# Optimization experiments

Hardware: AMD Instinct MI355X
Metric: run time of the kernel (lower is better)

Reference implementation:

```python
import jax, jax.numpy as jnp
import numpy as np

BS, N, D_ENT, K, D_IN, D_F, H, L, S = 128, 512, 256, 128, 1024, 256, 128, 2, 64
MAX_ENTITY_NUM = 512.0
TEMP = 1.0
NEG = -1e9


def _ln(x, g, b, eps=1e-5):
    m = jnp.mean(x, -1, keepdims=True)
    v = jnp.mean((x - m) ** 2, -1, keepdims=True)
    return (x - m) * jax.lax.rsqrt(v + eps) * g + b


def setup_inputs() -> dict:
    key = jax.random.key(0)
    ks = jax.random.split(key, 16)
    nrm = lambda k, sh, s=0.02: jax.random.normal(k, sh, jnp.float32) * s
    entity_num = jax.random.randint(ks[0], (BS,), 64, N)
    selected_units = jax.random.randint(ks[1], (BS, S), 0, N + 1) % (entity_num[:, None] + 1)
    selected_units_num = jax.random.randint(ks[2], (BS,), 1, S + 1).at[0].set(S)  # max == S so torch seq_len == S
    return dict(
        embedding=nrm(ks[3], (BS, D_IN), 1.0),
        entity_embedding=nrm(ks[4], (BS, N, D_ENT), 1.0),
        key_w=nrm(ks[5], (K, D_ENT)), key_b=jnp.zeros((K,), jnp.float32),
        q1_w=nrm(ks[6], (D_F, D_IN)), q1_b=jnp.zeros((D_F,), jnp.float32),
        q2_w=nrm(ks[7], (K, D_F)), q2_b=jnp.zeros((K,), jnp.float32),
        e1_w=nrm(ks[8], (D_F, K)), e1_b=jnp.zeros((D_F,), jnp.float32),
        e2_w=nrm(ks[9], (D_IN, D_F)), e2_b=jnp.zeros((D_IN,), jnp.float32),
        end_embedding=nrm(ks[10], (1, K), 0.09),
        lstm_wih=nrm(ks[11], (L, 4 * H, K)),
        lstm_whh=nrm(ks[12], (L, 4 * H, H)),
        ln_ig=jnp.ones((L, 4 * H), jnp.float32), ln_ib=jnp.zeros((L, 4 * H), jnp.float32),
        ln_hg=jnp.ones((L, 4 * H), jnp.float32), ln_hb=jnp.zeros((L, 4 * H), jnp.float32),
        ln_cg=jnp.ones((L, H), jnp.float32), ln_cb=jnp.zeros((L, H), jnp.float32),
        entity_num=entity_num, selected_units=selected_units, selected_units_num=selected_units_num,
    )


def _forward(embedding, entity_embedding, key_w, key_b, q1_w, q1_b, q2_w, q2_b,
             e1_w, e1_b, e2_w, e2_b, end_embedding, lstm_wih, lstm_whh,
             ln_ig, ln_ib, ln_hg, ln_hb, ln_cg, ln_cb,
             entity_num, selected_units, selected_units_num):
    bs = embedding.shape[0]
    ar = jnp.arange(bs)
    # keys: [bs, N+1, K] with end-embedding placed at position entity_num
    key = jnp.einsum('bnd,kd->bnk', entity_embedding, key_w) + key_b
    key = jnp.concatenate([key, jnp.zeros((bs, 1, K), key.dtype)], axis=1)
    key = key.at[ar, entity_num].set(end_embedding[0])
    # entity_reduce_type == 'constant': key_embeddings = embed_mlp(key / MAX_ENTITY_NUM)
    kr = key / MAX_ENTITY_NUM
    key_emb = jax.nn.relu(jnp.einsum('bnk,fk->bnf', kr, e1_w) + e1_b)
    key_emb = jnp.einsum('bnf,df->bnd', key_emb, e2_w) + e2_b  # [bs, N+1, D_IN]
    # precompute per-step masks (cumulative disabling of previously selected units;
    # end token blocked only at step 0, then re-enabled unless selected)
    init_mask = jnp.arange(N + 1)[None, :] < (entity_num + 1)[:, None]
    oh = jax.nn.one_hot(selected_units, N + 1, dtype=jnp.int32)
    prev = jnp.cumsum(oh, axis=1) - oh  # selected strictly before step i
    mask_seq = init_mask[:, None, :] & (prev == 0)  # [bs, S, N+1]
    mask_seq = mask_seq.at[ar, 0, entity_num].set(False)

    def step(carry, xs):
        ae, hs, cs = carry
        i, su_i, m_i = xs
        # query MLP
        x = jax.nn.relu(ae @ q1_w.T + q1_b) @ q2_w.T + q2_b  # [bs, K]
        new_hs, new_cs = [], []
        for l in range(L):  # layer-norm LSTM stack
            gates = _ln(x @ lstm_wih[l].T, ln_ig[l], ln_ib[l]) + _ln(hs[l] @ lstm_whh[l].T, ln_hg[l], ln_hb[l])
            ig, fg, gg, og = jnp.split(gates, 4, axis=-1)
            c = _ln(jax.nn.sigmoid(fg) * cs[l] + jax.nn.sigmoid(ig) * jnp.tanh(gg), ln_cg[l], ln_cb[l])
            h = jax.nn.sigmoid(og) * jnp.tanh(c)
            new_hs.append(h); new_cs.append(c)
            x = h
        logits = jnp.where(m_i, jnp.einsum('bk,bnk->bn', x, key) / TEMP, NEG)
        gate = ((i + 1) <= selected_units_num) & (su_i != entity_num)
        ae = ae + key_emb[ar, su_i] * gate[:, None].astype(ae.dtype)
        return (ae, jnp.stack(new_hs), jnp.stack(new_cs)), logits

    hs0 = jnp.zeros((L, bs, H), embedding.dtype)
    cs0 = jnp.zeros((L, bs, H), embedding.dtype)
    (ae, _, _), logits = jax.lax.scan(
        step, (embedding, hs0, cs0),
        (jnp.arange(S), selected_units.T, jnp.swapaxes(mask_seq, 0, 1)))
    return jnp.swapaxes(logits, 0, 1), ae  # logits [bs, S, N+1]


def reference(embedding, entity_embedding, key_w, key_b, q1_w, q1_b, q2_w, q2_b,
              e1_w, e1_b, e2_w, e2_b, end_embedding, lstm_wih, lstm_whh,
              ln_ig, ln_ib, ln_hg, ln_hb, ln_cg, ln_cb,
              entity_num, selected_units, selected_units_num):
    logits, ae = _forward(embedding, entity_embedding, key_w, key_b, q1_w, q1_b, q2_w, q2_b,
                          e1_w, e1_b, e2_w, e2_b, end_embedding, lstm_wih, lstm_whh,
                          ln_ig, ln_ib, ln_hg, ln_hb, ln_cg, ln_cb,
                          entity_num, selected_units, selected_units_num)
    # torch forward returns (logits, units=None, embedding, selected_units_num); units omitted here
    return logits, ae, selected_units_num
```

## Files before the change

### kernel.cpp

```cpp
#include <hip/hip_runtime.h>
#include <hip/hip_bf16.h>
#include <math.h>

#define BSZ   128
#define NENT  512
#define NP1   513
#define DENT  256
#define KDIM  128
#define DIN   1024
#define DF    256
#define HDIM  128
#define SSTEP 64
#define G4    512
#define NEGV  (-1e9f)
#define INV_MAX (1.0f/512.0f)

typedef float v2f __attribute__((ext_vector_type(2)));
typedef __attribute__((ext_vector_type(8))) short bf16x8;
typedef __attribute__((ext_vector_type(4))) float f32x4;

__device__ inline float sigf(float x){ return 1.f/(1.f+__expf(-x)); }
__device__ inline float tanh_fast(float x){ float e=__expf(2.f*x); return 1.f - 2.f/(e+1.f); }

__device__ inline float sum16_partial(float x){
  x += __int_as_float(__builtin_amdgcn_update_dpp(0, __float_as_int(x), 0x111, 0xf, 0xf, true));
  x += __int_as_float(__builtin_amdgcn_update_dpp(0, __float_as_int(x), 0x112, 0xf, 0xf, true));
  x += __int_as_float(__builtin_amdgcn_update_dpp(0, __float_as_int(x), 0x114, 0xf, 0xf, true));
  x += __int_as_float(__builtin_amdgcn_update_dpp(0, __float_as_int(x), 0x118, 0xf, 0xf, true));
  return x;
}
__device__ inline float wave_sum_partial(float x){
  x = sum16_partial(x);
  x += __int_as_float(__builtin_amdgcn_update_dpp(0, __float_as_int(x), 0x142, 0xa, 0xf, true));
  x += __int_as_float(__builtin_amdgcn_update_dpp(0, __float_as_int(x), 0x143, 0xc, 0xf, true));
  return x;
}
__device__ inline float wave_sum(float x){
  return __int_as_float(__builtin_amdgcn_readlane(__float_as_int(wave_sum_partial(x)), 63));
}

__device__ inline unsigned pk8(float4 f){
  int r = 0;
  r = __builtin_amdgcn_cvt_pk_fp8_f32(f.x, f.y, r, false);
  r = __builtin_amdgcn_cvt_pk_fp8_f32(f.z, f.w, r, true);
  return (unsigned)r;
}
__device__ inline float dot4_fp8(unsigned w, float4 h, float acc){
  v2f p = __builtin_amdgcn_cvt_pk_f32_fp8((int)w, false);
  acc = fmaf(p.x, h.x, acc); acc = fmaf(p.y, h.y, acc);
  p = __builtin_amdgcn_cvt_pk_f32_fp8((int)w, true);
  acc = fmaf(p.x, h.z, acc); acc = fmaf(p.y, h.w, acc);
  return acc;
}

__device__ inline float2 block_reduce2(float x, float y, float* red){
  float sx0 = wave_sum_partial(x), sy0 = wave_sum_partial(y);
  int w = threadIdx.x>>6;
  __syncthreads();
  if((threadIdx.x&63)==63){ red[w]=sx0; red[8+w]=sy0; }
  __syncthreads();
  float sx=0.f, sy=0.f;
  #pragma unroll
  for(int q=0;q<8;q++){ sx+=red[q]; sy+=red[8+q]; }
  return make_float2(sx,sy);
}

template<bool BKMAJOR, bool RELU, bool GATHER>
__global__ __launch_bounds__(256)
void mfma_gemm(const float* __restrict__ A, const float* __restrict__ B,
               const float* __restrict__ bias, float* __restrict__ C,
               int M, int N, int K,
               const int* __restrict__ gidx, float scale){
  __shared__ ushort Abf[64][72];
  __shared__ ushort Bbf[64][72];
  const int t = threadIdx.x;
  const int bm = blockIdx.x, bn = blockIdx.y;
  const int w = t>>6, l = t&63;
  const int lm = l&15, lg = l>>4;
  const int r0 = w*16;
  f32x4 acc[4];
  #pragma unroll
  for(int f=0;f<4;f++) acc[f] = (f32x4){0.f,0.f,0.f,0.f};

  for(int k0=0;k0<K;k0+=64){
    #pragma unroll
    for(int i=0;i<4;i++){
      int idx = t + i*256;
      int row = idx>>4, c4 = (idx&15)<<2;
      const float* src;
      if(GATHER){
        int gr = bm*64+row;
        src = &A[((size_t)(gr>>6)*NP1 + gidx[gr])*(size_t)K + k0 + c4];
      } else {
        src = &A[((size_t)bm*64+row)*K + k0 + c4];
      }
      float4 v = *(const float4*)src;
      if(GATHER){ v.x*=scale; v.y*=scale; v.z*=scale; v.w*=scale; }
      ushort4 u;
      u.x = __float_as_uint(v.x)>>16; u.y = __float_as_uint(v.y)>>16;
      u.z = __float_as_uint(v.z)>>16; u.w = __float_as_uint(v.w)>>16;
      *(ushort4*)&Abf[row][c4] = u;
    }
    if(!BKMAJOR){
      #pragma unroll
      for(int i=0;i<4;i++){
        int idx = t + i*256;
        int row = idx>>4, c4 = (idx&15)<<2;
        float4 v = *(const float4*)&B[((size_t)bn*64+row)*K + k0 + c4];
        ushort4 u;
        u.x = __float_as_uint(v.x)>>16; u.y = __float_as_uint(v.y)>>16;
        u.z = __float_as_uint(v.z)>>16; u.w = __float_as_uint(v.w)>>16;
        *(ushort4*)&Bbf[row][c4] = u;
      }
    } else {
      #pragma unroll
      for(int i=0;i<4;i++){
        int idx = t + i*256;
        int kr = idx>>4, n4 = (idx&15)<<2;
        float4 v = *(const float4*)&B[(size_t)(k0+kr)*N + bn*64 + n4];
        Bbf[n4+0][kr] = __float_as_uint(v.x)>>16;
        Bbf[n4+1][kr] = __float_as_uint(v.y)>>16;
        Bbf[n4+2][kr] = __float_as_uint(v.z)>>16;
        Bbf[n4+3][kr] = __float_as_uint(v.w)>>16;
      }
    }
    __syncthreads();
    #pragma unroll
    for(int kk=0;kk<64;kk+=32){
      bf16x8 a = *(const bf16x8*)&Abf[r0+lm][kk + lg*8];
      #pragma unroll
      for(int f=0;f<4;f++){
        bf16x8 b = *(const bf16x8*)&Bbf[f*16+lm][kk + lg*8];
        acc[f] = __builtin_amdgcn_mfma_f32_16x16x32_bf16(a, b, acc[f], 0,0,0);
      }
    }
    __syncthreads();
  }
  #pragma unroll
  for(int f=0;f<4;f++){
    int gcol = bn*64 + f*16 + lm;
    float bb = bias ? bias[gcol] : 0.f;
    #pragma unroll
    for(int r=0;r<4;r++){
      int grow = bm*64 + r0 + lg*4 + r;
      float v = acc[f][r] + bb;
      if(RELU) v = fmaxf(v, 0.f);
      C[(size_t)grow*N + gcol] = v;
    }
  }
}

__global__ __launch_bounds__(256)
void key_gemm_mfma(const float* __restrict__ A, const float* __restrict__ W,
                   const float* __restrict__ bias, const int* __restrict__ en,
                   const float* __restrict__ end_emb, float* __restrict__ C){
  __shared__ ushort Abf[64][264];
  __shared__ ushort Bbf[128][264];
  __shared__ float bs[128];
  const int t = threadIdx.x;
  const int bm = blockIdx.x;
  #pragma unroll
  for(int i=0;i<16;i++){
    int idx = t + i*256;
    int row = idx>>6, c4 = (idx&63)<<2;
    float4 v = *(const float4*)&A[((size_t)bm*64+row)*256 + c4];
    ushort4 u;
    u.x = __float_as_uint(v.x)>>16; u.y = __float_as_uint(v.y)>>16;
    u.z = __float_as_uint(v.z)>>16; u.w = __float_as_uint(v.w)>>16;
    *(ushort4*)&Abf[row][c4] = u;
  }
  #pragma unroll
  for(int i=0;i<32;i++){
    int idx = t + i*256;
    int row = idx>>6, c4 = (idx&63)<<2;
    float4 v = *(const float4*)&W[(size_t)row*256 + c4];
    ushort4 u;
    u.x = __float_as_uint(v.x)>>16; u.y = __float_as_uint(v.y)>>16;
    u.z = __float_as_uint(v.z)>>16; u.w = __float_as_uint(v.w)>>16;
    *(ushort4*)&Bbf[row][c4] = u;
  }
  if(t<128) bs[t] = bias[t];
  __syncthreads();
  const int w = t>>6, l = t&63;
  const int lm = l&15, lg = l>>4;
  const int r0 = w*16;
  f32x4 acc[8];
  #pragma unroll
  for(int f=0;f<8;f++) acc[f] = (f32x4){0.f,0.f,0.f,0.f};
  #pragma unroll
  for(int k0=0;k0<256;k0+=32){
    bf16x8 a = *(const bf16x8*)&Abf[r0+lm][k0 + lg*8];
    #pragma unroll
    for(int f=0;f<8;f++){
      bf16x8 b = *(const bf16x8*)&Bbf[f*16+lm][k0 + lg*8];
      acc[f] = __builtin_amdgcn_mfma_f32_16x16x32_bf16(a, b, acc[f], 0,0,0);
    }
  }
  #pragma unroll
  for(int f=0;f<8;f++){
    int gcol = f*16 + lm;
    float bb = bs[gcol];
    float ev = end_emb[gcol];
    #pragma unroll
    for(int r=0;r<4;r++){
      int grow = bm*64 + r0 + lg*4 + r;
      int bq = grow>>9, n = grow&511;
      size_t orow = (size_t)bq*NP1 + n;
      float v = acc[f][r] + bb;
      if(n == en[bq]) v = ev;
      C[orow*KDIM + gcol] = v;
    }
  }
}

__global__ __launch_bounds__(256)
void g0_gemm_ln(const float* __restrict__ X, const float* __restrict__ W,
                const float* __restrict__ gam, const float* __restrict__ bet,
                float* __restrict__ G0){
  __shared__ ushort Abf[16][136];
  __shared__ float redS[16][4], redQ[16][4];
  const int t = threadIdx.x, bm = blockIdx.x;
  const int w = t>>6, l = t&63, lm = l&15, lg = l>>4;
  {
    int idx = t*8;
    int row = idx>>7, c = idx&127;
    const float* src = &X[((size_t)bm*16+row)*128 + c];
    float4 a = *(const float4*)src;
    float4 d = *(const float4*)(src+4);
    ushort4 u0, u1;
    u0.x=__float_as_uint(a.x)>>16; u0.y=__float_as_uint(a.y)>>16;
    u0.z=__float_as_uint(a.z)>>16; u0.w=__float_as_uint(a.w)>>16;
    u1.x=__float_as_uint(d.x)>>16; u1.y=__float_as_uint(d.y)>>16;
    u1.z=__float_as_uint(d.z)>>16; u1.w=__float_as_uint(d.w)>>16;
    *(ushort4*)&Abf[row][c] = u0;
    *(ushort4*)&Abf[row][c+4] = u1;
  }
  __syncthreads();
  f32x4 acc[8];
  #pragma unroll
  for(int f=0;f<8;f++) acc[f] = (f32x4){0.f,0.f,0.f,0.f};
  #pragma unroll
  for(int kt=0;kt<4;kt++){
    int k0 = kt*32;
    bf16x8 a = *(const bf16x8*)&Abf[lm][k0 + lg*8];
    #pragma unroll
    for(int f=0;f<8;f++){
      int brow = w*128 + f*16 + lm;
      const float* bp = &W[(size_t)brow*128 + k0 + lg*8];
      float4 b0 = *(const float4*)bp;
      float4 b1 = *(const float4*)(bp+4);
      bf16x8 bfr;
      bfr[0]=(short)(__float_as_uint(b0.x)>>16); bfr[1]=(short)(__float_as_uint(b0.y)>>16);
      bfr[2]=(short)(__float_as_uint(b0.z)>>16); bfr[3]=(short)(__float_as_uint(b0.w)>>16);
      bfr[4]=(short)(__float_as_uint(b1.x)>>16); bfr[5]=(short)(__float_as_uint(b1.y)>>16);
      bfr[6]=(short)(__float_as_uint(b1.z)>>16); bfr[7]=(short)(__float_as_uint(b1.w)>>16);
      acc[f] = __builtin_amdgcn_mfma_f32_16x16x32_bf16(a, bfr, acc[f], 0,0,0);
    }
  }
  float mu[4], rs[4];
  #pragma unroll
  for(int r=0;r<4;r++){
    float s=0.f, q=0.f;
    #pragma unroll
    for(int f=0;f<8;f++){ float x=acc[f][r]; s+=x; q+=x*x; }
    s = sum16_partial(s);
    q = sum16_partial(q);
    if(lm==15){ redS[lg*4+r][w]=s; redQ[lg*4+r][w]=q; }
  }
  __syncthreads();
  #pragma unroll
  for(int r=0;r<4;r++){
    int row = lg*4+r;
    float S = redS[row][0]+redS[row][1]+redS[row][2]+redS[row][3];
    float Q = redQ[row][0]+redQ[row][1]+redQ[row][2]+redQ[row][3];
    mu[r] = S*(1.f/512.f);
    rs[r] = rsqrtf(Q*(1.f/512.f) - mu[r]*mu[r] + 1e-5f);
  }
  #pragma unroll
  for(int f=0;f<8;f++){
    int col = w*128 + f*16 + lm;
    float g = gam[col], bt = bet[col];
    #pragma unroll
    for(int r=0;r<4;r++){
      int grow = bm*16 + lg*4 + r;
      G0[(size_t)grow*G4 + col] = (acc[f][r]-mu[r])*rs[r]*g + bt;
    }
  }
}

__global__ __launch_bounds__(256)
void c0_kernel(const float* __restrict__ q1_w, const float* __restrict__ e2_b,
               float* __restrict__ c0v){
  __shared__ float red[4];
  int f = blockIdx.x, t = threadIdx.x;
  float4 a = *(const float4*)&q1_w[(size_t)f*DIN + t*4];
  float4 e = *(const float4*)&e2_b[t*4];
  float p = a.x*e.x + a.y*e.y + a.z*e.z + a.w*e.w;
  float s = wave_sum_partial(p);
  if((t&63)==63) red[t>>6] = s;
  __syncthreads();
  if(t==0) c0v[f] = red[0]+red[1]+red[2]+red[3];
}

__global__ void prefix_kernel(const float* __restrict__ U0, const float* __restrict__ Q1K,
                              const float* __restrict__ c0v, const float* __restrict__ T1,
                              const int* __restrict__ su, const int* __restrict__ en,
                              const int* __restrict__ sun,
                              float* __restrict__ RU, float* __restrict__ s1,
                              float* __restrict__ ngout){
  int b = blockIdx.x, f = threadIdx.x;
  float acc = U0[b*DF+f];
  float c0f = c0v[f];
  float s1a = 0.f, ng = 0.f;
  int enb = en[b], sunb = sun[b];
  for(int j=0;j<SSTEP;j++){
    int r = b*SSTEP+j;
    float q = Q1K[(size_t)r*DF+f];
    float tt = T1[(size_t)r*DF+f];
    RU[(size_t)r*DF+f] = fmaxf(acc,0.f);
    int sj = su[r];
    float g = ((j+1)<=sunb && sj!=enb) ? 1.f : 0.f;
    acc = fmaf(g, q + c0f, acc);
    s1a = fmaf(g, tt, s1a);
    ng += g;
  }
  s1[b*DF+f]=s1a;
  if(f==0) ngout[b]=ng;
}

__global__ __launch_bounds__(512)
__attribute__((amdgpu_waves_per_eu(2,2)))
void lstm_serial(const float* __restrict__ wih, const float* __restrict__ whh,
                 const float* __restrict__ G0,
                 const float* __restrict__ ln_ig, const float* __restrict__ ln_ib,
                 const float* __restrict__ ln_hg, const float* __restrict__ ln_hb,
                 const float* __restrict__ ln_cg, const float* __restrict__ ln_cb,
                 float* __restrict__ H1){
  const int b = blockIdx.x;
  const int j = threadIdx.x;
  __shared__ uint4 W0s8[8][512];
  __shared__ uint4 W1s8[8][512];
  __shared__ float h0s[128], h1s[128];
  __shared__ float pvv[512], pv1[512];
  __shared__ float lnA[512], lnB[512], lnC[512], lnD[512], lnE[512], lnF[512];
  __shared__ float red[32];

  #pragma unroll
  for(int c=0;c<8;c++){
    const float* s0 = &whh[(size_t)j*KDIM + c*16];
    uint4 p;
    p.x = pk8(*(const float4*)(s0+ 0));
    p.y = pk8(*(const float4*)(s0+ 4));
    p.z = pk8(*(const float4*)(s0+ 8));
    p.w = pk8(*(const float4*)(s0+12));
    W0s8[c][j] = p;
    const float* s1 = &wih[65536 + (size_t)j*KDIM + c*16];
    uint4 q;
    q.x = pk8(*(const float4*)(s1+ 0));
    q.y = pk8(*(const float4*)(s1+ 4));
    q.z = pk8(*(const float4*)(s1+ 8));
    q.w = pk8(*(const float4*)(s1+12));
    W1s8[c][j] = q;
  }
  uint4 w2p[8];
  #pragma unroll
  for(int c=0;c<8;c++){
    const float* s2 = &whh[65536 + (size_t)j*KDIM + c*16];
    w2p[c].x = pk8(*(const float4*)(s2+ 0));
    w2p[c].y = pk8(*(const float4*)(s2+ 4));
    w2p[c].z = pk8(*(const float4*)(s2+ 8));
    w2p[c].w = pk8(*(const float4*)(s2+12));
  }
  lnA[j] = ln_hg[j];     lnB[j] = ln_hb[j];
  lnC[j] = ln_ig[512+j]; lnD[j] = ln_ib[512+j];
  lnE[j] = ln_hg[512+j]; lnF[j] = ln_hb[512+j];

  float cg0A=0.f,cb0A=0.f,cg0B=0.f,cb0B=0.f;
  float cg1A=0.f,cb1A=0.f,cg1B=0.f,cb1B=0.f;
  float c0rA=0.f,c0rB=0.f,c1rA=0.f,c1rB=0.f;
  if(j<64){
    cg0A=ln_cg[j];      cb0A=ln_cb[j];
    cg0B=ln_cg[j+64];   cb0B=ln_cb[j+64];
    cg1A=ln_cg[128+j];    cb1A=ln_cb[128+j];
    cg1B=ln_cg[128+j+64]; cb1B=ln_cb[128+j+64];
  }
  if(j<128){ h0s[j]=0.f; h1s[j]=0.f; }
  __syncthreads();

  const float4* h04 = (const float4*)h0s;
  const float4* h14 = (const float4*)h1s;
  const int w = j>>6;

  for(int i=0;i<SSTEP;i++){
    float g0a[4], g0b[4];
    if(j<64){
      const float* gp = &G0[((size_t)b*SSTEP+i)*G4];
      #pragma unroll
      for(int k=0;k<4;k++){ g0a[k]=gp[j+128*k]; g0b[k]=gp[j+64+128*k]; }
    }

    float v = 0.f, vb = 0.f;
    #pragma unroll
    for(int c=0;c<8;c++){
      uint4 ww = W0s8[c][j];
      v  = dot4_fp8(ww.x, h04[4*c+0], v );
      vb = dot4_fp8(ww.y, h04[4*c+1], vb);
      v  = dot4_fp8(ww.z, h04[4*c+2], v );
      vb = dot4_fp8(ww.w, h04[4*c+3], vb);
    }
    v += vb;
    float v1 = 0.f, v1b = 0.f;
    #pragma unroll
    for(int c=0;c<8;c++){
      uint4 ww = w2p[c];
      v1  = dot4_fp8(ww.x, h14[4*c+0], v1 );
      v1b = dot4_fp8(ww.y, h14[4*c+1], v1b);
      v1  = dot4_fp8(ww.z, h14[4*c+2], v1 );
      v1b = dot4_fp8(ww.w, h14[4*c+3], v1b);
    }
    v1 += v1b;
    {
      float a  = wave_sum_partial(v);
      float bq = wave_sum_partial(v*v);
      float c2 = wave_sum_partial(v1);
      float d  = wave_sum_partial(v1*v1);
      if((j&63)==63){ red[w]=a; red[8+w]=bq; red[16+w]=c2; red[24+w]=d; }
    }
    pvv[j]=v; pv1[j]=v1;
    __syncthreads();

    if(j<64){
      float S=0.f,S2=0.f;
      #pragma unroll
      for(int q=0;q<8;q++){ S+=red[q]; S2+=red[8+q]; }
      float mu = S*(1.f/512.f);
      float rs = rsqrtf(S2*(1.f/512.f) - mu*mu + 1e-5f);
      float ashA[4], ashB[4];
      #pragma unroll
      for(int k=0;k<4;k++){
        int ia = j + 128*k, ib = j + 64 + 128*k;
        ashA[k] = g0a[k] + (pvv[ia]-mu)*rs*lnA[ia] + lnB[ia];
        ashB[k] = g0b[k] + (pvv[ib]-mu)*rs*lnA[ib] + lnB[ib];
      }
      float cpA = sigf(ashA[1])*c0rA + sigf(ashA[0])*tanh_fast(ashA[2]);
      float cpB = sigf(ashB[1])*c0rB + sigf(ashB[0])*tanh_fast(ashB[2]);
      float s  = wave_sum(cpA+cpB);
      float s2 = wave_sum(cpA*cpA+cpB*cpB);
      float muc = s*(1.f/128.f);
      float rsc = rsqrtf(s2*(1.f/128.f) - muc*muc + 1e-5f);
      c0rA = (cpA-muc)*rsc*cg0A + cb0A;
      c0rB = (cpB-muc)*rsc*cg0B + cb0B;
      h0s[j]    = sigf(ashA[3])*tanh_fast(c0rA);
      h0s[j+64] = sigf(ashB[3])*tanh_fast(c0rB);
    }
    __syncthreads();

    float u = 0.f, ub = 0.f;
    #pragma unroll
    for(int c=0;c<8;c++){
      uint4 ww = W1s8[c][j];
      u  = dot4_fp8(ww.x, h04[4*c+0], u );
      ub = dot4_fp8(ww.y, h04[4*c+1], ub);
      u  = dot4_fp8(ww.z, h04[4*c+2], u );
      ub = dot4_fp8(ww.w, h04[4*c+3], ub);
    }
    u += ub;
    {
      float a  = wave_sum_partial(u);
      float bq = wave_sum_partial(u*u);
      if((j&63)==63){ red[w]=a; red[8+w]=bq; }
    }
    pvv[j]=u;
    __syncthreads();

    if(j<64){
      float Su=0.f,Su2=0.f,Sv=0.f,Sv2=0.f;
      #pragma unroll
      for(int q=0;q<8;q++){ Su+=red[q]; Su2+=red[8+q]; Sv+=red[16+q]; Sv2+=red[24+q]; }
      float muu = Su*(1.f/512.f);
      float rsu = rsqrtf(Su2*(1.f/512.f) - muu*muu + 1e-5f);
      float muv = Sv*(1.f/512.f);
      float rsv = rsqrtf(Sv2*(1.f/512.f) - muv*muv + 1e-5f);
      float ashA[4], ashB[4];
      #pragma unroll
      for(int k=0;k<4;k++){
        int ia = j + 128*k, ib = j + 64 + 128*k;
        ashA[k] = (pvv[ia]-muu)*rsu*lnC[ia] + lnD[ia]
                + (pv1[ia]-muv)*rsv*lnE[ia] + lnF[ia];
        ashB[k] = (pvv[ib]-muu)*rsu*lnC[ib] + lnD[ib]
                + (pv1[ib]-muv)*rsv*lnE[ib] + lnF[ib];
      }
      float cpA = sigf(ashA[1])*c1rA + sigf(ashA[0])*tanh_fast(ashA[2]);
      float cpB = sigf(ashB[1])*c1rB + sigf(ashB[0])*tanh_fast(ashB[2]);
      float s  = wave_sum(cpA+cpB);
      float s2 = wave_sum(cpA*cpA+cpB*cpB);
      float muc = s*(1.f/128.f);
      float rsc = rsqrtf(s2*(1.f/128.f) - muc*muc + 1e-5f);
      c1rA = (cpA-muc)*rsc*cg1A + cb1A;
      c1rB = (cpB-muc)*rsc*cg1B + cb1B;
      float hA = sigf(ashA[3])*tanh_fast(c1rA);
      float hB = sigf(ashB[3])*tanh_fast(c1rB);
      h1s[j]    = hA;
      h1s[j+64] = hB;
      H1[((size_t)b*SSTEP+i)*HDIM + j]      = hA;
      H1[((size_t)b*SSTEP+i)*HDIM + j + 64] = hB;
    }
    __syncthreads();
  }
}

__global__ __launch_bounds__(512)
void logits_kernel(const float* __restrict__ key, const float* __restrict__ H1,
                   const int* __restrict__ en, const int* __restrict__ su,
                   float* __restrict__ out){
  const int b = blockIdx.x;
  const int ihalf = blockIdx.y;
  __shared__ float HsT[128][36];
  __shared__ int firstsel[NP1];
  for(int t=threadIdx.x; t<32*HDIM; t+=512){
    int il = t>>7, k = t&127;
    HsT[k][il] = H1[(size_t)b*SSTEP*HDIM + (size_t)(ihalf*32+il)*HDIM + k];
  }
  for(int t=threadIdx.x; t<NP1; t+=512) firstsel[t] = 1<<30;
  __syncthreads();
  if(threadIdx.x < SSTEP) atomicMin(&firstsel[su[b*SSTEP+threadIdx.x]], (int)threadIdx.x);
  __syncthreads();
  const int enb = en[b];
  const int tn = threadIdx.x & 255;
  const int ig = threadIdx.x >> 8;
  const int i0l = ig*16;
  const int ig0 = ihalf*32 + i0l;
  float acc0[16], acc1[16];
  #pragma unroll
  for(int q=0;q<16;q++){ acc0[q]=0.f; acc1[q]=0.f; }
  const float* kr0 = key + ((size_t)b*NP1 + tn)*KDIM;
  const float* kr1 = key + ((size_t)b*NP1 + tn + 256)*KDIM;
  for(int k=0;k<KDIM;k+=4){
    float4 kv0 = *(const float4*)&kr0[k];
    float4 kv1 = *(const float4*)&kr1[k];
    float k0a[4] = {kv0.x,kv0.y,kv0.z,kv0.w};
    float k1a[4] = {kv1.x,kv1.y,kv1.z,kv1.w};
    #pragma unroll
    for(int kk=0;kk<4;kk++){
      float4 h0 = *(const float4*)&HsT[k+kk][i0l+0];
      float4 h1 = *(const float4*)&HsT[k+kk][i0l+4];
      float4 h2 = *(const float4*)&HsT[k+kk][i0l+8];
      float4 h3 = *(const float4*)&HsT[k+kk][i0l+12];
      float ka = k0a[kk], kb = k1a[kk];
      acc0[ 0]=fmaf(ka,h0.x,acc0[ 0]); acc0[ 1]=fmaf(ka,h0.y,acc0[ 1]);
      acc0[ 2]=fmaf(ka,h0.z,acc0[ 2]); acc0[ 3]=fmaf(ka,h0.w,acc0[ 3]);
      acc0[ 4]=fmaf(ka,h1.x,acc0[ 4]); acc0[ 5]=fmaf(ka,h1.y,acc0[ 5]);
      acc0[ 6]=fmaf(ka,h1.z,acc0[ 6]); acc0[ 7]=fmaf(ka,h1.w,acc0[ 7]);
      acc0[ 8]=fmaf(ka,h2.x,acc0[ 8]); acc0[ 9]=fmaf(ka,h2.y,acc0[ 9]);
      acc0[10]=fmaf(ka,h2.z,acc0[10]); acc0[11]=fmaf(ka,h2.w,acc0[11]);
      acc0[12]=fmaf(ka,h3.x,acc0[12]); acc0[13]=fmaf(ka,h3.y,acc0[13]);
      acc0[14]=fmaf(ka,h3.z,acc0[14]); acc0[15]=fmaf(ka,h3.w,acc0[15]);
      acc1[ 0]=fmaf(kb,h0.x,acc1[ 0]); acc1[ 1]=fmaf(kb,h0.y,acc1[ 1]);
      acc1[ 2]=fmaf(kb,h0.z,acc1[ 2]); acc1[ 3]=fmaf(kb,h0.w,acc1[ 3]);
      acc1[ 4]=fmaf(kb,h1.x,acc1[ 4]); acc1[ 5]=fmaf(kb,h1.y,acc1[ 5]);
      acc1[ 6]=fmaf(kb,h1.z,acc1[ 6]); acc1[ 7]=fmaf(kb,h1.w,acc1[ 7]);
      acc1[ 8]=fmaf(kb,h2.x,acc1[ 8]); acc1[ 9]=fmaf(kb,h2.y,acc1[ 9]);
      acc1[10]=fmaf(kb,h2.z,acc1[10]); acc1[11]=fmaf(kb,h2.w,acc1[11]);
      acc1[12]=fmaf(kb,h3.x,acc1[12]); acc1[13]=fmaf(kb,h3.y,acc1[13]);
      acc1[14]=fmaf(kb,h3.z,acc1[14]); acc1[15]=fmaf(kb,h3.w,acc1[15]);
    }
  }
  const int n0 = tn, n1 = tn + 256;
  const int fs0 = firstsel[n0], fs1 = firstsel[n1];
  #pragma unroll
  for(int q=0;q<16;q++){
    int i = ig0 + q;
    bool m0 = (n0 <= enb) && (fs0 >= i) && !(i==0 && n0==enb);
    bool m1 = (n1 <= enb) && (fs1 >= i) && !(i==0 && n1==enb);
    out[((size_t)b*SSTEP + i)*NP1 + n0] = m0 ? acc0[q] : NEGV;
    out[((size_t)b*SSTEP + i)*NP1 + n1] = m1 ? acc1[q] : NEGV;
  }
  if(threadIdx.x < 32){
    int i = ihalf*32 + threadIdx.x;
    out[((size_t)b*SSTEP + i)*NP1 + 512] = NEGV;
  }
}

__global__ __launch_bounds__(256)
void ae_gemm(const float* __restrict__ A, const float* __restrict__ B,
             const float* __restrict__ emb, const float* __restrict__ e2_b,
             const float* __restrict__ ng, const int* __restrict__ sun,
             float* __restrict__ out){
  const size_t AE_OFF = (size_t)BSZ*SSTEP*NP1;
  const size_t SUN_OFF = AE_OFF + (size_t)BSZ*DIN;
  __shared__ ushort Abf[64][72];
  __shared__ ushort Bbf[64][72];
  const int t = threadIdx.x;
  const int bm = blockIdx.x, bn = blockIdx.y;
  const int w = t>>6, l = t&63;
  const int lm = l&15, lg = l>>4;
  const int r0 = w*16;
  f32x4 acc[4];
  #pragma unroll
  for(int f=0;f<4;f++) acc[f] = (f32x4){0.f,0.f,0.f,0.f};
  for(int k0=0;k0<256;k0+=64){
    #pragma unroll
    for(int i=0;i<4;i++){
      int idx = t + i*256;
      int row = idx>>4, c4 = (idx&15)<<2;
      float4 v = *(const float4*)&A[((size_t)bm*64+row)*256 + k0 + c4];
      ushort4 u;
      u.x = __float_as_uint(v.x)>>16; u.y = __float_as_uint(v.y)>>16;
      u.z = __float_as_uint(v.z)>>16; u.w = __float_as_uint(v.w)>>16;
      *(ushort4*)&Abf[row][c4] = u;
    }
    #pragma unroll
    for(int i=0;i<4;i++){
      int idx = t + i*256;
      int row = idx>>4, c4 = (idx&15)<<2;
      float4 v = *(const float4*)&B[((size_t)bn*64+row)*256 + k0 + c4];
      ushort4 u;
      u.x = __float_as_uint(v.x)>>16; u.y = __float_as_uint(v.y)>>16;
      u.z = __float_as_uint(v.z)>>16; u.w = __float_as_uint(v.w)>>16;
      *(ushort4*)&Bbf[row][c4] = u;
    }
    __syncthreads();
    #pragma unroll
    for(int kk=0;kk<64;kk+=32){
      bf16x8 a = *(const bf16x8*)&Abf[r0+lm][kk + lg*8];
      #pragma unroll
      for(int f=0;f<4;f++){
        bf16x8 b = *(const bf16x8*)&Bbf[f*16+lm][kk + lg*8];
        acc[f] = __builtin_amdgcn_mfma_f32_16x16x32_bf16(a, b, acc[f], 0,0,0);
      }
    }
    __syncthreads();
  }
  #pragma unroll
  for(int f=0;f<4;f++){
    int gcol = bn*64 + f*16 + lm;
    float eb = e2_b[gcol];
    #pragma unroll
    for(int r=0;r<4;r++){
      int grow = bm*64 + r0 + lg*4 + r;
      size_t o = (size_t)grow*DIN + gcol;
      out[AE_OFF + o] = emb[o] + acc[f][r] + ng[grow]*eb;
    }
  }
  if(bm==0 && bn==0 && t<BSZ) out[SUN_OFF + t] = (float)sun[t];
}

extern "C" void kernel_launch(void* const* d_in, const int* in_sizes, int n_in,
                              void* d_out, int out_size, void* d_ws, size_t ws_size,
                              hipStream_t stream){
  const float* emb     = (const float*)d_in[0];
  const float* ent     = (const float*)d_in[1];
  const float* key_w   = (const float*)d_in[2];
  const float* key_b   = (const float*)d_in[3];
  const float* q1_w    = (const float*)d_in[4];
  const float* q1_b    = (const float*)d_in[5];
  const float* q2_w    = (const float*)d_in[6];
  const float* q2_b    = (const float*)d_in[7];
  const float* e1_w    = (const float*)d_in[8];
  const float* e1_b    = (const float*)d_in[9];
  const float* e2_w    = (const float*)d_in[10];
  const float* e2_b    = (const float*)d_in[11];
  const float* end_emb = (const float*)d_in[12];
  const float* wih     = (const float*)d_in[13];
  const float* whh     = (const float*)d_in[14];
  const float* ln_ig   = (const float*)d_in[15];
  const float* ln_ib   = (const float*)d_in[16];
  const float* ln_hg   = (const float*)d_in[17];
  const float* ln_hb   = (const float*)d_in[18];
  const float* ln_cg   = (const float*)d_in[19];
  const float* ln_cb   = (const float*)d_in[20];
  const int* en  = (const int*)d_in[21];
  const int* su  = (const int*)d_in[22];
  const int* sun = (const int*)d_in[23];
  float* out = (float*)d_out;
  float* ws  = (float*)d_ws;

  const size_t o_key = 0;
  const size_t o_T1  = o_key + 8404992;
  const size_t o_q1e = o_T1  + 2097152;
  const size_t o_c0  = o_q1e + 65536;
  const size_t o_U0  = o_c0  + 1024;
  const size_t o_Q1K = o_U0  + 32768;
  const size_t o_RU  = o_Q1K + 2097152;
  const size_t o_X   = o_RU  + 2097152;
  const size_t o_G0  = o_X   + 1048576;
  const size_t o_s1  = o_G0  + 4194304;
  const size_t o_ng  = o_s1  + 32768;
  const size_t o_H1  = o_ng  + 1024;

  key_gemm_mfma<<<1024,256,0,stream>>>(ent, key_w, key_b, en, end_emb, ws+o_key);
  mfma_gemm<false,true,true><<<dim3(128,4),256,0,stream>>>(ws+o_key, e1_w, e1_b, ws+o_T1,
                                                           8192,256,128, su, INV_MAX);
  mfma_gemm<true,false,false><<<dim3(4,4),256,0,stream>>>(q1_w, e2_w, nullptr, ws+o_q1e,
                                                          256,256,1024, nullptr, 1.f);
  c0_kernel<<<256,256,0,stream>>>(q1_w, e2_b, ws+o_c0);
  mfma_gemm<false,false,false><<<dim3(2,4),256,0,stream>>>(emb, q1_w, q1_b, ws+o_U0,
                                                           128,256,1024, nullptr, 1.f);
  mfma_gemm<false,false,false><<<dim3(128,4),256,0,stream>>>(ws+o_T1, ws+o_q1e, nullptr, ws+o_Q1K,
                                                             8192,256,256, nullptr, 1.f);
  prefix_kernel<<<128,256,0,stream>>>(ws+o_U0, ws+o_Q1K, ws+o_c0, ws+o_T1, su, en, sun,
                                      ws+o_RU, ws+o_s1, ws+o_ng);
  mfma_gemm<false,false,false><<<dim3(128,2),256,0,stream>>>(ws+o_RU, q2_w, q2_b, ws+o_X,
                                                             8192,128,256, nullptr, 1.f);
  g0_gemm_ln<<<512,256,0,stream>>>(ws+o_X, wih, ln_ig, ln_ib, ws+o_G0);
  lstm_serial<<<128,512,0,stream>>>(wih, whh, ws+o_G0,
                                    ln_ig, ln_ib, ln_hg, ln_hb, ln_cg, ln_cb, ws+o_H1);
  logits_kernel<<<dim3(128,2),512,0,stream>>>(ws+o_key, ws+o_H1, en, su, out);
  ae_gemm<<<dim3(2,16),256,0,stream>>>(ws+o_s1, e2_w, emb, e2_b, ws+o_ng, sun, out);
}
```

Before: 529.7 us.

## Use fp8 MFMA for serial LSTM recurrent matvecs with fp8 hidden state

Replaces the per-thread scalar fp8 dot products in the serial LSTM kernel with 16x16x32 fp8 MFMA instructions. The hidden vector is quantized to fp8 and placed in row 0 of the A operand, with the other rows zeroed. Weights are re-laid out in shared memory and registers to match the MFMA B-operand fragments. The goal is fewer VALU ops on the latency-bound recurrent step. In exchange, 15 of 16 MFMA rows are wasted, and quantizing the hidden state to fp8 lowers accuracy.

```diff
diff --git a/kernel.cpp b/kernel.cpp
--- a/kernel.cpp
+++ b/kernel.cpp
@@ -18,6 +18,7 @@
 typedef float v2f __attribute__((ext_vector_type(2)));
 typedef __attribute__((ext_vector_type(8))) short bf16x8;
 typedef __attribute__((ext_vector_type(4))) float f32x4;
+typedef long i64;
 
 __device__ inline float sigf(float x){ return 1.f/(1.f+__expf(-x)); }
 __device__ inline float tanh_fast(float x){ float e=__expf(2.f*x); return 1.f - 2.f/(e+1.f); }
@@ -45,13 +46,7 @@
   r = __builtin_amdgcn_cvt_pk_fp8_f32(f.z, f.w, r, true);
   return (unsigned)r;
 }
-__device__ inline float dot4_fp8(unsigned w, float4 h, float acc){
-  v2f p = __builtin_amdgcn_cvt_pk_f32_fp8((int)w, false);
-  acc = fmaf(p.x, h.x, acc); acc = fmaf(p.y, h.y, acc);
-  p = __builtin_amdgcn_cvt_pk_f32_fp8((int)w, true);
-  acc = fmaf(p.x, h.z, acc); acc = fmaf(p.y, h.w, acc);
-  return acc;
-}
+__device__ inline i64 u2l(uint2 v){ union{uint2 u; i64 l;} x; x.u=v; return x.l; }
 
 __device__ inline float2 block_reduce2(float x, float y, float* red){
   float sx0 = wave_sum_partial(x), sy0 = wave_sum_partial(y);
@@ -338,38 +333,43 @@
                  float* __restrict__ H1){
   const int b = blockIdx.x;
   const int j = threadIdx.x;
-  __shared__ uint4 W0s8[8][512];
-  __shared__ uint4 W1s8[8][512];
-  __shared__ float h0s[128], h1s[128];
+  const int w = j>>6, l = j&63;
+  const int lm = l&15, lg = l>>4;
+  __shared__ uint2 W0f[4][4][512];
+  __shared__ uint2 W1f[4][4][512];
+  __shared__ uint4 h0q8[8], h1q8[8];
   __shared__ float pvv[512], pv1[512];
   __shared__ float lnA[512], lnB[512], lnC[512], lnD[512], lnE[512], lnF[512];
   __shared__ float red[32];
 
-  #pragma unroll
-  for(int c=0;c<8;c++){
-    const float* s0 = &whh[(size_t)j*KDIM + c*16];
-    uint4 p;
-    p.x = pk8(*(const float4*)(s0+ 0));
-    p.y = pk8(*(const float4*)(s0+ 4));
-    p.z = pk8(*(const float4*)(s0+ 8));
-    p.w = pk8(*(const float4*)(s0+12));
-    W0s8[c][j] = p;
-    const float* s1 = &wih[65536 + (size_t)j*KDIM + c*16];
-    uint4 q;
-    q.x = pk8(*(const float4*)(s1+ 0));
-    q.y = pk8(*(const float4*)(s1+ 4));
-    q.z = pk8(*(const float4*)(s1+ 8));
-    q.w = pk8(*(const float4*)(s1+12));
-    W1s8[c][j] = q;
-  }
-  uint4 w2p[8];
-  #pragma unroll
-  for(int c=0;c<8;c++){
-    const float* s2 = &whh[65536 + (size_t)j*KDIM + c*16];
-    w2p[c].x = pk8(*(const float4*)(s2+ 0));
-    w2p[c].y = pk8(*(const float4*)(s2+ 4));
-    w2p[c].z = pk8(*(const float4*)(s2+ 8));
-    w2p[c].w = pk8(*(const float4*)(s2+12));
+  {
+    unsigned dw[32];
+    #pragma unroll
+    for(int q=0;q<32;q++) dw[q] = pk8(*(const float4*)&whh[(size_t)j*KDIM + q*4]);
+    #pragma unroll
+    for(int kt=0;kt<4;kt++)
+      #pragma unroll
+      for(int g=0;g<4;g++)
+        W0f[kt][g][j] = make_uint2(dw[kt*8+g*2], dw[kt*8+g*2+1]);
+    #pragma unroll
+    for(int q=0;q<32;q++) dw[q] = pk8(*(const float4*)&wih[65536 + (size_t)j*KDIM + q*4]);
+    #pragma unroll
+    for(int kt=0;kt<4;kt++)
+      #pragma unroll
+      for(int g=0;g<4;g++)
+        W1f[kt][g][j] = make_uint2(dw[kt*8+g*2], dw[kt*8+g*2+1]);
+  }
+  uint2 w2f[4][4];
+  #pragma unroll
+  for(int c=0;c<4;c++){
+    int row = w*64 + c*16 + lm;
+    #pragma unroll
+    for(int kt=0;kt<4;kt++){
+      int k0 = kt*32 + lg*8;
+      float4 x0 = *(const float4*)&whh[65536 + (size_t)row*KDIM + k0];
+      float4 x1 = *(const float4*)&whh[65536 + (size_t)row*KDIM + k0 + 4];
+      w2f[c][kt] = make_uint2(pk8(x0), pk8(x1));
+    }
   }
   lnA[j] = ln_hg[j];     lnB[j] = ln_hb[j];
   lnC[j] = ln_ig[512+j]; lnD[j] = ln_ib[512+j];
@@ -384,12 +384,10 @@
     cg1A=ln_cg[128+j];    cb1A=ln_cb[128+j];
     cg1B=ln_cg[128+j+64]; cb1B=ln_cb[128+j+64];
   }
-  if(j<128){ h0s[j]=0.f; h1s[j]=0.f; }
-  __syncthreads();
-
-  const float4* h04 = (const float4*)h0s;
-  const float4* h14 = (const float4*)h1s;
-  const int w = j>>6;
+  if(j<8){ h0q8[j]=(uint4){0,0,0,0}; h1q8[j]=(uint4){0,0,0,0}; }
+  __syncthreads();
+
+  const int colbase = w*64;
 
   for(int i=0;i<SSTEP;i++){
     float g0a[4], g0b[4];
@@ -399,34 +397,43 @@
       for(int k=0;k<4;k++){ g0a[k]=gp[j+128*k]; g0b[k]=gp[j+64+128*k]; }
     }
 
-    float v = 0.f, vb = 0.f;
-    #pragma unroll
-    for(int c=0;c<8;c++){
-      uint4 ww = W0s8[c][j];
-      v  = dot4_fp8(ww.x, h04[4*c+0], v );
-      vb = dot4_fp8(ww.y, h04[4*c+1], vb);
-      v  = dot4_fp8(ww.z, h04[4*c+2], v );
-      vb = dot4_fp8(ww.w, h04[4*c+3], vb);
-    }
-    v += vb;
-    float v1 = 0.f, v1b = 0.f;
-    #pragma unroll
-    for(int c=0;c<8;c++){
-      uint4 ww = w2p[c];
-      v1  = dot4_fp8(ww.x, h14[4*c+0], v1 );
-      v1b = dot4_fp8(ww.y, h14[4*c+1], v1b);
-      v1  = dot4_fp8(ww.z, h14[4*c+2], v1 );
-      v1b = dot4_fp8(ww.w, h14[4*c+3], v1b);
-    }
-    v1 += v1b;
+    f32x4 accv[4], acc1[4];
+    #pragma unroll
+    for(int c=0;c<4;c++){ accv[c]=(f32x4){0.f,0.f,0.f,0.f}; acc1[c]=(f32x4){0.f,0.f,0.f,0.f}; }
+    #pragma unroll
+    for(int kt=0;kt<4;kt++){
+      uint2 a0 = make_uint2(0,0), a1 = make_uint2(0,0);
+      if(lm==0){
+        a0 = *(const uint2*)((const char*)h0q8 + kt*32 + lg*8);
+        a1 = *(const uint2*)((const char*)h1q8 + kt*32 + lg*8);
+      }
+      i64 A0 = u2l(a0), A1 = u2l(a1);
+      #pragma unroll
+      for(int c=0;c<4;c++){
+        accv[c] = __builtin_amdgcn_mfma_f32_16x16x32_fp8_fp8(A0, u2l(W0f[kt][lg][colbase+c*16+lm]), accv[c], 0,0,0);
+        acc1[c] = __builtin_amdgcn_mfma_f32_16x16x32_fp8_fp8(A1, u2l(w2f[c][kt]), acc1[c], 0,0,0);
+      }
+    }
     {
-      float a  = wave_sum_partial(v);
-      float bq = wave_sum_partial(v*v);
-      float c2 = wave_sum_partial(v1);
-      float d  = wave_sum_partial(v1*v1);
-      if((j&63)==63){ red[w]=a; red[8+w]=bq; red[16+w]=c2; red[24+w]=d; }
-    }
-    pvv[j]=v; pv1[j]=v1;
+      float sv=0.f, sq=0.f, s1v=0.f, s1q=0.f;
+      #pragma unroll
+      for(int c=0;c<4;c++){
+        float x = accv[c][0]; sv += x; sq += x*x;
+        float y = acc1[c][0]; s1v += y; s1q += y*y;
+      }
+      float a  = wave_sum_partial(sv);
+      float bq = wave_sum_partial(sq);
+      float c2 = wave_sum_partial(s1v);
+      float d  = wave_sum_partial(s1q);
+      if(l==63){ red[w]=a; red[8+w]=bq; red[16+w]=c2; red[24+w]=d; }
+      if(l<16){
+        #pragma unroll
+        for(int c=0;c<4;c++){
+          pvv[colbase + c*16 + l] = accv[c][0];
+          pv1[colbase + c*16 + l] = acc1[c][0];
+        }
+      }
+    }
     __syncthreads();
 
     if(j<64){
@@ -450,27 +457,38 @@
       float rsc = rsqrtf(s2*(1.f/128.f) - muc*muc + 1e-5f);
       c0rA = (cpA-muc)*rsc*cg0A + cb0A;
       c0rB = (cpB-muc)*rsc*cg0B + cb0B;
-      h0s[j]    = sigf(ashA[3])*tanh_fast(c0rA);
-      h0s[j+64] = sigf(ashB[3])*tanh_fast(c0rB);
+      float hA = sigf(ashA[3])*tanh_fast(c0rA);
+      float hB = sigf(ashB[3])*tanh_fast(c0rB);
+      ((unsigned char*)h0q8)[j]    = (unsigned char)(__builtin_amdgcn_cvt_pk_fp8_f32(hA,hA,0,false)&0xff);
+      ((unsigned char*)h0q8)[j+64] = (unsigned char)(__builtin_amdgcn_cvt_pk_fp8_f32(hB,hB,0,false)&0xff);
     }
     __syncthreads();
 
-    float u = 0.f, ub = 0.f;
-    #pragma unroll
-    for(int c=0;c<8;c++){
-      uint4 ww = W1s8[c][j];
-      u  = dot4_fp8(ww.x, h04[4*c+0], u );
-      ub = dot4_fp8(ww.y, h04[4*c+1], ub);
-      u  = dot4_fp8(ww.z, h04[4*c+2], u );
-      ub = dot4_fp8(ww.w, h04[4*c+3], ub);
-    }
-    u += ub;
+    f32x4 accu[4];
+    #pragma unroll
+    for(int c=0;c<4;c++) accu[c]=(f32x4){0.f,0.f,0.f,0.f};
+    #pragma unroll
+    for(int kt=0;kt<4;kt++){
+      uint2 a0 = make_uint2(0,0);
+      if(lm==0) a0 = *(const uint2*)((const char*)h0q8 + kt*32 + lg*8);
+      i64 A0 = u2l(a0);
+      #pragma unroll
+      for(int c=0;c<4;c++){
+        accu[c] = __builtin_amdgcn_mfma_f32_16x16x32_fp8_fp8(A0, u2l(W1f[kt][lg][colbase+c*16+lm]), accu[c], 0,0,0);
+      }
+    }
     {
-      float a  = wave_sum_partial(u);
-      float bq = wave_sum_partial(u*u);
-      if((j&63)==63){ red[w]=a; red[8+w]=bq; }
-    }
-    pvv[j]=u;
+      float su=0.f, squ=0.f;
+      #pragma unroll
+      for(int c=0;c<4;c++){ float x=accu[c][0]; su+=x; squ+=x*x; }
+      float a  = wave_sum_partial(su);
+      float bq = wave_sum_partial(squ);
+      if(l==63){ red[w]=a; red[8+w]=bq; }
+      if(l<16){
+        #pragma unroll
+        for(int c=0;c<4;c++) pvv[colbase + c*16 + l] = accu[c][0];
+      }
+    }
     __syncthreads();
 
     if(j<64){
@@ -500,8 +518,8 @@
       c1rB = (cpB-muc)*rsc*cg1B + cb1B;
       float hA = sigf(ashA[3])*tanh_fast(c1rA);
       float hB = sigf(ashB[3])*tanh_fast(c1rB);
-      h1s[j]    = hA;
-      h1s[j+64] = hB;
+      ((unsigned char*)h1q8)[j]    = (unsigned char)(__builtin_amdgcn_cvt_pk_fp8_f32(hA,hA,0,false)&0xff);
+      ((unsigned char*)h1q8)[j+64] = (unsigned char)(__builtin_amdgcn_cvt_pk_fp8_f32(hB,hB,0,false)&0xff);
       H1[((size_t)b*SSTEP+i)*HDIM + j]      = hA;
       H1[((size_t)b*SSTEP+i)*HDIM + j + 64] = hB;
     }
```

After: 440.3 us, median of 2. 16.9% less time.
